# Optimization experiments

Measured on AMD Instinct MI355X. Metric: run time of the kernel, lower is better.

## Reference

```python
import jax, jax.numpy as jnp
from jax import lax
import numpy as np

B, T, H, A, C = 32, 4096, 512, 512, 32  # batch, enc frames, hidden, attn_size, conv_size


def setup_inputs() -> dict:
    key = jax.random.key(0)
    ks = jax.random.split(key, 10)
    return {
        "decoder_output": jax.random.normal(ks[0], (B, 1, H), jnp.float32),
        "encoder_outputs": jax.random.normal(ks[1], (B, T, H), jnp.float32),
        "last_alignment": jax.random.uniform(ks[2], (B, T), jnp.float32),
        "conv_w": jax.random.normal(ks[3], (C, 1, 3), jnp.float32) * 0.1,   # Conv1d(1->C, k=3)
        "conv_b": jax.random.normal(ks[4], (C,), jnp.float32) * 0.1,
        "W": jax.random.normal(ks[5], (A, H), jnp.float32) * (1.0 / np.sqrt(H)),
        "V": jax.random.normal(ks[6], (A, H), jnp.float32) * (1.0 / np.sqrt(H)),
        "U": jax.random.normal(ks[7], (A, C), jnp.float32) * (1.0 / np.sqrt(C)),
        "b": jax.random.uniform(ks[8], (A,), jnp.float32, -0.1, 0.1),
        "w": jax.random.normal(ks[9], (A,), jnp.float32) * (1.0 / np.sqrt(A)),
    }


def reference(decoder_output, encoder_outputs, last_alignment, conv_w, conv_b, W, V, U, b, w):
    # location conv: [B,1,T] -> [B,C,T], kernel 3, padding 1
    conv = lax.conv_general_dilated(
        last_alignment[:, None, :], conv_w,
        window_strides=(1,), padding=[(1, 1)],
        dimension_numbers=("NCH", "OIH", "NCH"))
    conv_feat = (conv + conv_b[None, :, None]).transpose(0, 2, 1)  # [B,T,C]

    dec_proj = jnp.einsum("blh,ah->bla", decoder_output, W)        # [B,1,A]
    enc_proj = jnp.einsum("bth,ah->bta", encoder_outputs, V)       # [B,T,A]
    loc_proj = jnp.einsum("btc,ac->bta", conv_feat, U)             # [B,T,A]

    scores = jnp.einsum("bta,a->bt", jnp.tanh(dec_proj + enc_proj + loc_proj + b), w)  # [B,T]
    alignment = jax.nn.softmax(scores, axis=-1)                    # [B,T]
    output = jnp.einsum("bt,bth->bh", alignment, encoder_outputs)  # [B,H]
    return output, alignment
```

## Files before the change

### kernel.cpp

```cpp
#include <hip/hip_runtime.h>
#include <hip/hip_bf16.h>

#define B_ 32
#define T_ 4096
#define H_ 512
#define A_ 512
#define C_ 32
#define KTOT 544
#define NKS  (KTOT / 32)
#define TT   64

typedef float f32x4 __attribute__((ext_vector_type(4)));
typedef __bf16 bf16x8 __attribute__((ext_vector_type(8)));

__device__ inline float fast_tanh(float x) {
    float t = __expf(2.0f * x);
    return 1.0f - 2.0f / (t + 1.0f);
}

__device__ __forceinline__ void async16(const void* g, void* l) {
    __builtin_amdgcn_global_load_lds(
        (const __attribute__((address_space(1))) unsigned int*)g,
        (__attribute__((address_space(3))) unsigned int*)l, 16, 0, 0);
}

__global__ __launch_bounds__(256) void prep_kernel(
    const float* __restrict__ dec, const float* __restrict__ W,
    const float* __restrict__ bvec, const float* __restrict__ V,
    const float* __restrict__ U,
    float* __restrict__ dpb, __bf16* __restrict__ Vsall) {
    int id = blockIdx.x * 256 + threadIdx.x;
    const int N1 = B_ * A_;
    const int N2 = A_ * H_;
    if (id < N1) {
        int b = id / A_, a = id % A_;
        const float* dr = dec + b * H_;
        const float* wr = W + (size_t)a * H_;
        float s = 0.f;
        #pragma unroll 8
        for (int h = 0; h < H_; ++h) s += dr[h] * wr[h];
        dpb[id] = s + bvec[a];
    } else if (id < N1 + N2) {
        int e = id - N1;
        int a = e >> 9, k = e & 511;
        Vsall[((k >> 3) * A_ + a) * 8 + (k & 7)] = (__bf16)V[(size_t)a * H_ + k];
    } else {
        int e = id - N1 - N2;
        int a = e >> 5, c = e & 31;
        int k = H_ + c;
        Vsall[((k >> 3) * A_ + a) * 8 + (k & 7)] = (__bf16)U[a * C_ + c];
    }
}

__global__ __launch_bounds__(512) void scores_mfma(
    const float* __restrict__ enc, const float* __restrict__ align,
    const float* __restrict__ conv_w, const float* __restrict__ conv_b,
    const __bf16* __restrict__ Vsall, const float* __restrict__ dpb,
    const float* __restrict__ wvec, float* __restrict__ scores) {
    const int t0 = blockIdx.x * TT;
    const int b  = blockIdx.y;
    const int tid = threadIdx.x;
    const int lane = tid & 63, wid = tid >> 6;
    const int row0 = lane & 15;
    const int kg   = lane >> 4;
    const int wq   = wid & 3;
    const int wr   = wid >> 2;
    const int wcol = wq * 128;

    __shared__ char smem[73728];
    float* spart = (float*)smem;

    const float* encb = enc + ((size_t)b * T_ + t0) * H_;
    const int arow = tid >> 2, akgl = tid & 3;

    {
        __bf16* bdst = (__bf16*)(smem + 8192);
        #pragma unroll
        for (int i = 0; i < 4; ++i) {
            int u = i * 512 + tid;
            async16(Vsall + u * 8, bdst + u * 8);
        }
    }
    if (tid < 256) {
        const float* p = encb + arow * H_ + akgl * 8;
        f32x4 lo = *reinterpret_cast<const f32x4*>(p);
        f32x4 hi = *reinterpret_cast<const f32x4*>(p + 4);
        bf16x8 v;
        v[0] = (__bf16)lo.x; v[1] = (__bf16)lo.y; v[2] = (__bf16)lo.z; v[3] = (__bf16)lo.w;
        v[4] = (__bf16)hi.x; v[5] = (__bf16)hi.y; v[6] = (__bf16)hi.z; v[7] = (__bf16)hi.w;
        int g = tid ^ ((tid >> 4) & 7);
        *reinterpret_cast<bf16x8*>((__bf16*)smem + g * 8) = v;
    }
    __syncthreads();

    f32x4 acc[2][8];
    #pragma unroll
    for (int m = 0; m < 2; ++m)
        #pragma unroll
        for (int n = 0; n < 8; ++n) acc[m][n] = (f32x4){0.f, 0.f, 0.f, 0.f};

    int cur = 0;
    for (int ks = 0; ks < NKS; ++ks) {
        __bf16* Acur = (__bf16*)(smem + (cur ? 4096 : 0));
        __bf16* Anxt = (__bf16*)(smem + (cur ? 0 : 4096));
        __bf16* Bcur = (__bf16*)(smem + 8192 + (cur ? 32768 : 0));
        __bf16* Bnxt = (__bf16*)(smem + 8192 + (cur ? 0 : 32768));

        f32x4 alo, ahi;
        bool stage = (ks + 1 < NKS);
        bool conv_step = (ks + 1 == NKS - 1);
        if (stage) {
            const __bf16* vchunk = Vsall + (size_t)(ks + 1) * (4 * A_ * 8);
            #pragma unroll
            for (int i = 0; i < 4; ++i) {
                int u = i * 512 + tid;
                async16(vchunk + u * 8, Bnxt + u * 8);
            }
            if (tid < 256 && !conv_step) {
                const float* p = encb + arow * H_ + (ks + 1) * 32 + akgl * 8;
                alo = *reinterpret_cast<const f32x4*>(p);
                ahi = *reinterpret_cast<const f32x4*>(p + 4);
            }
        }

        bf16x8 afrag[2];
        #pragma unroll
        for (int m = 0; m < 2; ++m) {
            int row = wr * 32 + m * 16 + row0;
            int u = row * 4 + kg;
            int g = u ^ ((u >> 4) & 7);
            afrag[m] = *reinterpret_cast<const bf16x8*>(Acur + g * 8);
        }
        const __bf16* bp = Bcur + kg * (A_ * 8);
        #pragma unroll
        for (int n = 0; n < 8; ++n) {
            bf16x8 bfrag = *reinterpret_cast<const bf16x8*>(bp + (wcol + n * 16 + row0) * 8);
            acc[0][n] = __builtin_amdgcn_mfma_f32_16x16x32_bf16(afrag[0], bfrag, acc[0][n], 0, 0, 0);
            acc[1][n] = __builtin_amdgcn_mfma_f32_16x16x32_bf16(afrag[1], bfrag, acc[1][n], 0, 0, 0);
        }

        if (stage && tid < 256) {
            bf16x8 v;
            if (!conv_step) {
                v[0] = (__bf16)alo.x; v[1] = (__bf16)alo.y; v[2] = (__bf16)alo.z; v[3] = (__bf16)alo.w;
                v[4] = (__bf16)ahi.x; v[5] = (__bf16)ahi.y; v[6] = (__bf16)ahi.z; v[7] = (__bf16)ahi.w;
            } else {
                int t = t0 + arow;
                float x0 = (t > 0) ? align[b * T_ + t - 1] : 0.f;
                float x1 = align[b * T_ + t];
                float x2 = (t + 1 < T_) ? align[b * T_ + t + 1] : 0.f;
                #pragma unroll
                for (int e = 0; e < 8; ++e) {
                    int c = akgl * 8 + e;
                    v[e] = (__bf16)(conv_b[c] + conv_w[c * 3 + 0] * x0
                                  + conv_w[c * 3 + 1] * x1 + conv_w[c * 3 + 2] * x2);
                }
            }
            int g = tid ^ ((tid >> 4) & 7);
            *reinterpret_cast<bf16x8*>(Anxt + g * 8) = v;
        }
        __syncthreads();
        cur ^= 1;
    }

    float dval[8], wv[8];
    #pragma unroll
    for (int n = 0; n < 8; ++n) {
        int a = wcol + n * 16 + row0;
        dval[n] = dpb[b * A_ + a];
        wv[n]   = wvec[a];
    }
    #pragma unroll
    for (int m = 0; m < 2; ++m) {
        float rs[4] = {0.f, 0.f, 0.f, 0.f};
        #pragma unroll
        for (int n = 0; n < 8; ++n) {
            #pragma unroll
            for (int j = 0; j < 4; ++j) {
                float x = acc[m][n][j] + dval[n];
                rs[j] += fast_tanh(x) * wv[n];
            }
        }
        #pragma unroll
        for (int j = 0; j < 4; ++j) {
            float v = rs[j];
            v += __shfl_xor(v, 1);
            v += __shfl_xor(v, 2);
            v += __shfl_xor(v, 4);
            v += __shfl_xor(v, 8);
            if (row0 == 0) spart[wq * TT + wr * 32 + m * 16 + kg * 4 + j] = v;
        }
    }
    __syncthreads();
    if (tid < TT) {
        float s = spart[0 * TT + tid] + spart[1 * TT + tid]
                + spart[2 * TT + tid] + spart[3 * TT + tid];
        scores[b * T_ + t0 + tid] = s;
    }
}

__global__ __launch_bounds__(256) void softmax_k(
    const float* __restrict__ scores, float* __restrict__ out_align) {
    int b = blockIdx.x;
    int tid = threadIdx.x;
    __shared__ float redm[4];
    __shared__ float reds[4];
    float local[16];
    float mx = -1e30f;
    #pragma unroll
    for (int i = 0; i < 16; ++i) {
        float s = scores[b * T_ + tid + i * 256];
        local[i] = s;
        mx = fmaxf(mx, s);
    }
    for (int off = 32; off >= 1; off >>= 1) mx = fmaxf(mx, __shfl_xor(mx, off));
    if ((tid & 63) == 0) redm[tid >> 6] = mx;
    __syncthreads();
    mx = fmaxf(fmaxf(redm[0], redm[1]), fmaxf(redm[2], redm[3]));
    float sum = 0.f;
    #pragma unroll
    for (int i = 0; i < 16; ++i) { local[i] = __expf(local[i] - mx); sum += local[i]; }
    for (int off = 32; off >= 1; off >>= 1) sum += __shfl_xor(sum, off);
    if ((tid & 63) == 0) reds[tid >> 6] = sum;
    __syncthreads();
    sum = reds[0] + reds[1] + reds[2] + reds[3];
    float inv = 1.0f / sum;
    #pragma unroll
    for (int i = 0; i < 16; ++i)
        out_align[b * T_ + tid + i * 256] = local[i] * inv;
}

__global__ __launch_bounds__(512) void pout_k(
    const float* __restrict__ enc, const float* __restrict__ alpha,
    float* __restrict__ pout) {
    int chunk = blockIdx.x;
    int b = blockIdx.y;
    int tid = threadIdx.x;
    int t0 = chunk * 512;
    __shared__ float as[512];
    as[tid] = alpha[b * T_ + t0 + tid];
    __syncthreads();
    float acc = 0.f;
    const float* ep = enc + ((size_t)b * T_ + t0) * H_ + tid;
    #pragma unroll 4
    for (int t = 0; t < 512; ++t) acc += as[t] * ep[(size_t)t * H_];
    pout[((size_t)b * 8 + chunk) * H_ + tid] = acc;
}

__global__ __launch_bounds__(512) void combine_k(
    const float* __restrict__ pout, float* __restrict__ out) {
    int b = blockIdx.x; int h = threadIdx.x;
    float s = 0.f;
    #pragma unroll
    for (int c = 0; c < 8; ++c) s += pout[((size_t)b * 8 + c) * H_ + h];
    out[b * H_ + h] = s;
}

extern "C" void kernel_launch(void* const* d_in, const int* in_sizes, int n_in,
                              void* d_out, int out_size, void* d_ws, size_t ws_size,
                              hipStream_t stream) {
    const float* dec    = (const float*)d_in[0];
    const float* enc    = (const float*)d_in[1];
    const float* align  = (const float*)d_in[2];
    const float* conv_w = (const float*)d_in[3];
    const float* conv_b = (const float*)d_in[4];
    const float* W      = (const float*)d_in[5];
    const float* V      = (const float*)d_in[6];
    const float* U      = (const float*)d_in[7];
    const float* bvec   = (const float*)d_in[8];
    const float* wvec   = (const float*)d_in[9];
    float* out       = (float*)d_out;
    float* out_align = out + B_ * H_;

    char* ws = (char*)d_ws;
    float*  dpb    = (float*)(ws);
    float*  scores = (float*)(ws + (64 << 10));
    float*  pout   = (float*)(ws + (576 << 10));
    __bf16* Vsall  = (__bf16*)(ws + (1088 << 10));

    prep_kernel<<<(B_ * A_ + A_ * H_ + A_ * C_) / 256, 256, 0, stream>>>(
        dec, W, bvec, V, U, dpb, Vsall);
    scores_mfma<<<dim3(T_ / TT, B_), 512, 0, stream>>>(enc, align, conv_w, conv_b,
                                                       Vsall, dpb, wvec, scores);
    softmax_k<<<B_, 256, 0, stream>>>(scores, out_align);
    pout_k<<<dim3(8, B_), 512, 0, stream>>>(enc, out_align, pout);
    combine_k<<<B_, 512, 0, stream>>>(pout, out);
}
```

Before: 199.9 us.

## Fuse weighted encoder sum into scores kernel via split-softmax partials

The scores kernel now computes a per-chunk local max, exp-sum and exp-weighted partial sum of encoder rows while the tile is likely still cached. The separate pout pass, which re-read the full encoder tensor from memory, is replaced by a combine kernel that rescales the per-chunk partials online-softmax style. This removes a second full read of the encoder tensor. In exchange it adds per-block epilogue work and a larger partial buffer (64 chunks per batch) that the combine step must read.

```diff
diff --git a/kernel.cpp b/kernel.cpp
--- a/kernel.cpp
+++ b/kernel.cpp
@@ -9,6 +9,7 @@
 #define KTOT 544
 #define NKS  (KTOT / 32)
 #define TT   64
+#define NCH  (T_ / TT)
 
 typedef float f32x4 __attribute__((ext_vector_type(4)));
 typedef __bf16 bf16x8 __attribute__((ext_vector_type(8)));
@@ -56,8 +57,10 @@
     const float* __restrict__ enc, const float* __restrict__ align,
     const float* __restrict__ conv_w, const float* __restrict__ conv_b,
     const __bf16* __restrict__ Vsall, const float* __restrict__ dpb,
-    const float* __restrict__ wvec, float* __restrict__ scores) {
-    const int t0 = blockIdx.x * TT;
+    const float* __restrict__ wvec, float* __restrict__ scores,
+    float* __restrict__ ml_buf, float* __restrict__ u_buf) {
+    const int bx = blockIdx.x;
+    const int t0 = bx * TT;
     const int b  = blockIdx.y;
     const int tid = threadIdx.x;
     const int lane = tid & 63, wid = tid >> 6;
@@ -69,6 +72,8 @@
 
     __shared__ char smem[73728];
     float* spart = (float*)smem;
+    float* eL    = (float*)(smem + 2048);
+    float* mbox  = (float*)(smem + 2560);
 
     const float* encb = enc + ((size_t)b * T_ + t0) * H_;
     const int arow = tid >> 2, akgl = tid & 3;
@@ -192,10 +197,37 @@
         }
     }
     __syncthreads();
+
     if (tid < TT) {
         float s = spart[0 * TT + tid] + spart[1 * TT + tid]
                 + spart[2 * TT + tid] + spart[3 * TT + tid];
         scores[b * T_ + t0 + tid] = s;
+        float mx = s;
+        #pragma unroll
+        for (int off = 32; off >= 1; off >>= 1) mx = fmaxf(mx, __shfl_xor(mx, off));
+        float e = __expf(s - mx);
+        eL[tid] = e;
+        float l = e;
+        #pragma unroll
+        for (int off = 32; off >= 1; off >>= 1) l += __shfl_xor(l, off);
+        if (tid == 0) {
+            mbox[0] = mx;
+            ml_buf[((size_t)b * NCH + bx) * 2 + 0] = mx;
+            ml_buf[((size_t)b * NCH + bx) * 2 + 1] = l;
+        }
+    }
+    __syncthreads();
+    {
+        float u0 = 0.f, u1 = 0.f, u2 = 0.f, u3 = 0.f;
+        const float* ep = encb + tid;
+        #pragma unroll 4
+        for (int t = 0; t < TT; t += 4) {
+            u0 += eL[t]     * ep[(size_t)t * H_];
+            u1 += eL[t + 1] * ep[(size_t)(t + 1) * H_];
+            u2 += eL[t + 2] * ep[(size_t)(t + 2) * H_];
+            u3 += eL[t + 3] * ep[(size_t)(t + 3) * H_];
+        }
+        u_buf[((size_t)b * NCH + bx) * H_ + tid] = (u0 + u1) + (u2 + u3);
     }
 }
 
@@ -230,30 +262,31 @@
         out_align[b * T_ + tid + i * 256] = local[i] * inv;
 }
 
-__global__ __launch_bounds__(512) void pout_k(
-    const float* __restrict__ enc, const float* __restrict__ alpha,
-    float* __restrict__ pout) {
-    int chunk = blockIdx.x;
-    int b = blockIdx.y;
-    int tid = threadIdx.x;
-    int t0 = chunk * 512;
-    __shared__ float as[512];
-    as[tid] = alpha[b * T_ + t0 + tid];
+__global__ __launch_bounds__(512) void combine2_k(
+    const float* __restrict__ ml_buf, const float* __restrict__ u_buf,
+    float* __restrict__ out) {
+    int b = blockIdx.x;
+    int h = threadIdx.x;
+    __shared__ float wsh[NCH];
+    __shared__ float dsh[1];
+    if (h < NCH) {
+        float m = ml_buf[((size_t)b * NCH + h) * 2];
+        float mb = m;
+        #pragma unroll
+        for (int off = 32; off >= 1; off >>= 1) mb = fmaxf(mb, __shfl_xor(mb, off));
+        float w = __expf(m - mb);
+        wsh[h] = w;
+        float d = w * ml_buf[((size_t)b * NCH + h) * 2 + 1];
+        #pragma unroll
+        for (int off = 32; off >= 1; off >>= 1) d += __shfl_xor(d, off);
+        if (h == 0) dsh[0] = d;
+    }
     __syncthreads();
     float acc = 0.f;
-    const float* ep = enc + ((size_t)b * T_ + t0) * H_ + tid;
     #pragma unroll 4
-    for (int t = 0; t < 512; ++t) acc += as[t] * ep[(size_t)t * H_];
-    pout[((size_t)b * 8 + chunk) * H_ + tid] = acc;
-}
-
-__global__ __launch_bounds__(512) void combine_k(
-    const float* __restrict__ pout, float* __restrict__ out) {
-    int b = blockIdx.x; int h = threadIdx.x;
-    float s = 0.f;
-    #pragma unroll
-    for (int c = 0; c < 8; ++c) s += pout[((size_t)b * 8 + c) * H_ + h];
-    out[b * H_ + h] = s;
+    for (int c = 0; c < NCH; ++c)
+        acc += wsh[c] * u_buf[((size_t)b * NCH + c) * H_ + h];
+    out[b * H_ + h] = acc / dsh[0];
 }
 
 extern "C" void kernel_launch(void* const* d_in, const int* in_sizes, int n_in,
@@ -275,14 +308,15 @@
     char* ws = (char*)d_ws;
     float*  dpb    = (float*)(ws);
     float*  scores = (float*)(ws + (64 << 10));
-    float*  pout   = (float*)(ws + (576 << 10));
-    __bf16* Vsall  = (__bf16*)(ws + (1088 << 10));
+    float*  ml_buf = (float*)(ws + (576 << 10));
+    float*  u_buf  = (float*)(ws + (592 << 10));
+    __bf16* Vsall  = (__bf16*)(ws + (592 << 10) + (4 << 20));
 
     prep_kernel<<<(B_ * A_ + A_ * H_ + A_ * C_) / 256, 256, 0, stream>>>(
         dec, W, bvec, V, U, dpb, Vsall);
     scores_mfma<<<dim3(T_ / TT, B_), 512, 0, stream>>>(enc, align, conv_w, conv_b,
-                                                       Vsall, dpb, wvec, scores);
+                                                       Vsall, dpb, wvec, scores,
+                                                       ml_buf, u_buf);
     softmax_k<<<B_, 256, 0, stream>>>(scores, out_align);
-    pout_k<<<dim3(8, B_), 512, 0, stream>>>(enc, out_align, pout);
-    combine_k<<<B_, 512, 0, stream>>>(pout, out);
-}
+    combine2_k<<<B_, 512, 0, stream>>>(ml_buf, u_buf, out);
+}
```

Measured after the change: 166.9 us. 1.2x faster.
